# Optimization experiments

Hardware: AMD Instinct MI355X
Metric: run time of the kernel (lower is better)

Reference implementation:

```python
import jax, jax.numpy as jnp
import numpy as np

N = 8192
D = 768
TEMPERATURE = 0.1
EPS_NORM = 1e-8   # torch CosineSimilarity eps
EPS_LOG = 1e-6


def setup_inputs() -> dict:
    key = jax.random.key(0)
    k1, k2, k3 = jax.random.split(key, 3)
    features = jax.random.normal(k1, (N, D), dtype=jnp.float32)
    positive_mask = jax.random.randint(k2, (N, N), 0, 2).astype(jnp.float32)
    negative_mask = jax.random.randint(k3, (N, N), 0, 2).astype(jnp.float32)
    return {"features": features, "positive_mask": positive_mask, "negative_mask": negative_mask}


def reference(features, positive_mask, negative_mask):
    n = features.shape[0]
    # cosine similarity: normalize then GEMM (same math as broadcasted CosineSimilarity)
    norms = jnp.linalg.norm(features, axis=1, keepdims=True)
    fn = features / jnp.maximum(norms, EPS_NORM)
    sim = jnp.exp(jnp.matmul(fn, fn.T) / TEMPERATURE)  # [N, N]
    # zero out self-contrast on the diagonal of both masks
    not_eye = 1.0 - jnp.eye(n, dtype=features.dtype)
    pm = positive_mask * not_eye
    nm = negative_mask * not_eye
    pos_sums = pm.sum(axis=1)
    pos_sums = jnp.where(pos_sums == 0, 1.0, pos_sums)
    neg = jnp.sum(sim * nm, axis=1, keepdims=True)  # [N, 1]
    log_prob = -jnp.log(sim / neg + EPS_LOG)        # [N, N]
    per_row = jnp.sum(log_prob * pm, axis=1) / pos_sums
    return jnp.mean(per_row)
```

## Files before the change

### kernel.cpp

```cpp
#include <hip/hip_runtime.h>
#include <hip/hip_bf16.h>

#define NROWS 8192
#define DDIM 768

typedef short short8 __attribute__((ext_vector_type(8)));
typedef float floatx4 __attribute__((ext_vector_type(4)));
typedef float f4 __attribute__((ext_vector_type(4)));
#define TSTRIDE 132

__global__ __launch_bounds__(256) void normalize_k(const float* __restrict__ f,
                                                   __hip_bfloat16* __restrict__ fn) {
    const int row = blockIdx.x;
    const int t = threadIdx.x;
    const float* fr = f + (size_t)row * DDIM;
    float v0 = fr[t];
    float v1 = fr[t + 256];
    float v2 = fr[t + 512];
    float ss = v0 * v0 + v1 * v1 + v2 * v2;
#pragma unroll
    for (int m = 32; m; m >>= 1) ss += __shfl_xor(ss, m, 64);
    __shared__ float wsum[4];
    if ((t & 63) == 0) wsum[t >> 6] = ss;
    __syncthreads();
    float tot = wsum[0] + wsum[1] + wsum[2] + wsum[3];
    float inv = 1.0f / fmaxf(sqrtf(tot), 1e-8f);
    __hip_bfloat16* o = fn + (size_t)row * DDIM;
    o[t]       = __float2bfloat16(v0 * inv);
    o[t + 256] = __float2bfloat16(v1 * inv);
    o[t + 512] = __float2bfloat16(v2 * inv);
}

__global__ __launch_bounds__(256, 3) void ntxent_main(
        const __hip_bfloat16* __restrict__ fn,
        const float* __restrict__ pmask, const float* __restrict__ nmask,
        float* __restrict__ negG, float* __restrict__ sG,
        float* __restrict__ pG) {
    __shared__ __align__(16) char smem[53248];
    __hip_bfloat16* Is = (__hip_bfloat16*)smem;
    __hip_bfloat16* Js = Is + 128 * 32;
    char* maskLds = smem + 16384;
    float* T = (float*)smem;

    const int t = threadIdx.x;
    const int lane = t & 63;
    const int wv = t >> 6;
    const int wm = wv & 1;
    const int wn = wv >> 1;
    const int q  = lane >> 4;
    const int cl = lane & 15;

    const int bt0 = blockIdx.x;
    const int bt = (bt0 & 7) * 260 + (bt0 >> 3);

    int r = (int)((sqrtf(8.0f * (float)bt + 1.0f) - 1.0f) * 0.5f);
    while ((r + 1) * (r + 2) / 2 <= bt) ++r;
    while (r * (r + 1) / 2 > bt) --r;
    const int c = bt - r * (r + 1) / 2;
    const int rowBase = c * 128;
    const int colBase = r * 128;
    const bool offDiag = (c != r);

    const int rdSw = ((q ^ ((cl >> 1) & 3)) << 4);

    const int sRow = t >> 5;
    const int sChunk = (t & 31) ^ (sRow & 7);

    floatx4 acc[4][4];
#pragma unroll
    for (int mf = 0; mf < 4; ++mf)
#pragma unroll
        for (int nf = 0; nf < 4; ++nf)
            acc[mf][nf] = (floatx4){0.f, 0.f, 0.f, 0.f};

    unsigned int dw[4] = {0u, 0u, 0u, 0u};
    unsigned int mw[4] = {0u, 0u, 0u, 0u};

    auto issue_slab = [&](int s) {
        const int slot = s % 9;
        const int side = s >> 5;
        const int rg   = (s & 31) >> 1;
        const float* mp = (s & 1) ? nmask : pmask;
        const int rowG = (side ? colBase : rowBase) + rg * 8 + sRow;
        const int colG = (side ? rowBase : colBase) + sChunk * 4;
        const float* src = mp + (size_t)rowG * NROWS + colG;
        __builtin_amdgcn_global_load_lds(
            (const __attribute__((address_space(1))) void*)src,
            (__attribute__((address_space(3))) void*)(maskLds + slot * 4096 + t * 16),
            16, 0, 0);
    };

    auto pack_slab = [&](int s) {
        const int slot = s % 9;
        const int side = s >> 5;
        const int rg   = (s & 31) >> 1;
        const int sh   = (s & 1) ? 16 : 0;
        if (side == 0) {
            if (wn == (rg >> 3) && (cl >> 3) == (rg & 1)) {
                const int nf = (rg >> 1) & 3;
                const int rl = cl & 7;
                const char* base = maskLds + slot * 4096 + rl * 512;
                float word = 0.f;
#pragma unroll
                for (int mf = 3; mf >= 0; --mf) {
                    const int pos = (wm * 16 + mf * 4 + q) ^ rl;
                    const f4 m = *(const f4*)(base + pos * 16);
                    float nib = fmaf(2.f, m[1], m[0]) + fmaf(8.f, m[3], 4.f * m[2]);
                    word = fmaf(word, 16.f, nib);
                }
                dw[nf] |= ((unsigned int)word) << sh;
            }
        } else if (offDiag) {
            if (wv == (rg & 3)) {
                const int st = rg >> 2;
                const int rl = (t >> 3) & 7;
                const int h  = t & 7;
                const char* base = maskLds + slot * 4096 + rl * 512;
                float word = 0.f;
#pragma unroll
                for (int u = 3; u >= 0; --u) {
                    const int pos = (h * 4 + u) ^ rl;
                    const f4 m = *(const f4*)(base + pos * 16);
                    float nib = fmaf(2.f, m[1], m[0]) + fmaf(8.f, m[3], 4.f * m[2]);
                    word = fmaf(word, 16.f, nib);
                }
                mw[st] |= ((unsigned int)word) << sh;
            }
        }
    };

    issue_slab(0); issue_slab(1); issue_slab(2);
    issue_slab(3); issue_slab(4); issue_slab(5);
    asm volatile("s_waitcnt vmcnt(3)" ::: "memory");

#pragma unroll
    for (int kt = 0; kt < 24; ++kt) {
        const int k0 = kt * 32;
        asm volatile("s_waitcnt lgkmcnt(0)\n\ts_barrier" ::: "memory");

#pragma unroll
        for (int it = 0; it < 2; ++it) {
            const int s = it * 256 + t;
            const int rr = s >> 2;
            const int cg = (s & 3) ^ ((rr >> 1) & 3);
            const __hip_bfloat16* ga = fn + (size_t)(rowBase + rr) * DDIM + k0 + cg * 8;
            const __hip_bfloat16* gb = fn + (size_t)(colBase + rr) * DDIM + k0 + cg * 8;
            __builtin_amdgcn_global_load_lds(
                (const __attribute__((address_space(1))) void*)ga,
                (__attribute__((address_space(3))) void*)((char*)Is + s * 16), 16, 0, 0);
            __builtin_amdgcn_global_load_lds(
                (const __attribute__((address_space(1))) void*)gb,
                (__attribute__((address_space(3))) void*)((char*)Js + s * 16), 16, 0, 0);
        }

#pragma unroll
        for (int gl = 0; gl < 3; ++gl) {
            const int s = 3 * (kt + 2) + gl;
            if (s <= 63) issue_slab(s);
        }

#pragma unroll
        for (int gl = 0; gl < 3; ++gl) {
            const int s = 3 * kt + gl;
            if (s <= 63) pack_slab(s);
        }

        if (kt <= 18)      asm volatile("s_waitcnt vmcnt(3)\n\ts_barrier" ::: "memory");
        else if (kt == 19) asm volatile("s_waitcnt vmcnt(1)\n\ts_barrier" ::: "memory");
        else               asm volatile("s_waitcnt vmcnt(0)\n\ts_barrier" ::: "memory");

        short8 if_[4];
#pragma unroll
        for (int nf = 0; nf < 4; ++nf) {
            const int rr = wn * 64 + nf * 16 + cl;
            if_[nf] = *(const short8*)((const char*)Is + rr * 64 + rdSw);
        }
#pragma unroll
        for (int mf = 0; mf < 4; ++mf) {
            const int rr = wm * 64 + mf * 16 + cl;
            const short8 jf = *(const short8*)((const char*)Js + rr * 64 + rdSw);
#pragma unroll
            for (int nf = 0; nf < 4; ++nf)
                acc[mf][nf] = __builtin_amdgcn_mfma_f32_16x16x32_bf16(
                    jf, if_[nf], acc[mf][nf], 0, 0, 0);
        }
    }

    const int col64 = colBase + wm * 64;
    const int jb0 = col64 + q * 4;
#pragma unroll
    for (int nf = 0; nf < 4; ++nf) {
        const int grow = rowBase + wn * 64 + nf * 16 + cl;
        const unsigned int w = dw[nf];
        float aN = 0.f, aS = 0.f, aP = 0.f;
#pragma unroll
        for (int mf = 0; mf < 4; ++mf) {
            const int jbase = jb0 + mf * 16;
#pragma unroll
            for (int reg = 0; reg < 4; ++reg) {
                const int b = mf * 4 + reg;
                float pmv = ((w >> b) & 1u) ? 1.0f : 0.0f;
                float nmv = ((w >> (16 + b)) & 1u) ? 1.0f : 0.0f;
                if (grow == jbase + reg) { pmv = 0.f; nmv = 0.f; }
                float v = acc[mf][nf][reg];
                float e = __builtin_amdgcn_exp2f(v * 14.4269504089f);
                aN = fmaf(nmv, e, aN);
                aS = fmaf(pmv, v, aS);
                aP += pmv;
            }
        }
        aN += __shfl_xor(aN, 16, 64);  aN += __shfl_xor(aN, 32, 64);
        aS += __shfl_xor(aS, 16, 64);  aS += __shfl_xor(aS, 32, 64);
        aP += __shfl_xor(aP, 16, 64);  aP += __shfl_xor(aP, 32, 64);
        if (q == 0) {
            atomicAdd(&negG[grow], aN);
            atomicAdd(&sG[grow],   aS);
            atomicAdd(&pG[grow],   aP);
        }
    }

    if (offDiag) {
        const int jl2 = t >> 3;
        const int iseg = (t & 7) * 16;
#pragma unroll
        for (int st = 0; st < 4; ++st) {
            __syncthreads();
            if (wm == (st >> 1)) {
#pragma unroll
                for (int m2 = 0; m2 < 2; ++m2) {
                    const int mf = (st & 1) * 2 + m2;
#pragma unroll
                    for (int nf = 0; nf < 4; ++nf) {
                        const int i = wn * 64 + nf * 16 + cl;
#pragma unroll
                        for (int reg = 0; reg < 4; ++reg) {
                            const int jl = m2 * 16 + q * 4 + reg;
                            T[jl * TSTRIDE + i] = acc[mf][nf][reg];
                        }
                    }
                }
            }
            __syncthreads();
            const int jg = colBase + st * 32 + jl2;
            const unsigned int w = mw[st];
            const f4* tv = (const f4*)(T + jl2 * TSTRIDE + iseg);
            float aN = 0.f, aS = 0.f, aP = 0.f;
#pragma unroll
            for (int u = 0; u < 4; ++u) {
                f4 v4 = tv[u];
#pragma unroll
                for (int e = 0; e < 4; ++e) {
                    const int b = u * 4 + e;
                    float v = v4[e];
                    float pmv = ((w >> b) & 1u) ? 1.0f : 0.0f;
                    float nmv = ((w >> (16 + b)) & 1u) ? 1.0f : 0.0f;
                    float ex = __builtin_amdgcn_exp2f(v * 14.4269504089f);
                    aN = fmaf(nmv, ex, aN);
                    aS = fmaf(pmv, v, aS);
                    aP += pmv;
                }
            }
            aN += __shfl_xor(aN, 1, 64); aN += __shfl_xor(aN, 2, 64); aN += __shfl_xor(aN, 4, 64);
            aS += __shfl_xor(aS, 1, 64); aS += __shfl_xor(aS, 2, 64); aS += __shfl_xor(aS, 4, 64);
            aP += __shfl_xor(aP, 1, 64); aP += __shfl_xor(aP, 2, 64); aP += __shfl_xor(aP, 4, 64);
            if ((t & 7) == 0) {
                atomicAdd(&negG[jg], aN);
                atomicAdd(&sG[jg],   aS);
                atomicAdd(&pG[jg],   aP);
            }
        }
    }
}

__global__ __launch_bounds__(1024) void final_k(const float* __restrict__ negG,
        const float* __restrict__ sG, const float* __restrict__ pG,
        float* __restrict__ out) {
    const int t = threadIdx.x;
    float sum = 0.f;
    for (int i = t; i < NROWS; i += 1024) {
        float P = pG[i];
        if (P > 0.f) {
            sum += (P * logf(negG[i]) - 10.0f * sG[i]) / P;
        }
    }
#pragma unroll
    for (int m = 32; m; m >>= 1) sum += __shfl_xor(sum, m, 64);
    __shared__ float wsum[16];
    if ((t & 63) == 0) wsum[t >> 6] = sum;
    __syncthreads();
    if (t < 16) {
        float v = wsum[t];
#pragma unroll
        for (int m = 8; m; m >>= 1) v += __shfl_xor(v, m, 16);
        if (t == 0) out[0] = v / (float)NROWS;
    }
}

extern "C" void kernel_launch(void* const* d_in, const int* in_sizes, int n_in,
                              void* d_out, int out_size, void* d_ws, size_t ws_size,
                              hipStream_t stream) {
    const float* feat  = (const float*)d_in[0];
    const float* pmask = (const float*)d_in[1];
    const float* nmask = (const float*)d_in[2];
    float* out = (float*)d_out;

    char* ws = (char*)d_ws;
    __hip_bfloat16* fn = (__hip_bfloat16*)ws;
    float* negG = (float*)(ws + 12582912);
    float* sG = negG + NROWS;
    float* pG = sG + NROWS;

    hipMemsetAsync(negG, 0, 3 * NROWS * sizeof(float), stream);

    normalize_k<<<NROWS, 256, 0, stream>>>(feat, fn);

    ntxent_main<<<2080, 256, 0, stream>>>(fn, pmask, nmask, negG, sG, pG);

    final_k<<<1, 1024, 0, stream>>>(negG, sG, pG, out);
}
```

Baseline: 573.4 us.

## Enlarge symmetric tiles to 256x256 with 512-thread blocks and rebalanced mask pipeline

Each block now covers a 256x256 tile of the upper-triangular similarity matrix instead of 128x128. It uses 8 waves, larger accumulators (4x8 MFMA fragments per wave) and a 128KB LDS footprint. The mask slab prefetch schedule is reworked to spread 128 slabs evenly over the 24 K-steps through a 12-slot ring, and slab packing now runs after the MFMAs. The aim is to halve per-tile feature reloads and cut the block count and atomic traffic. The cost is fewer blocks (528), only 2 per CU at most, and heavier register and LDS pressure, which may hurt latency hiding and load balance.

```diff
diff --git a/kernel.cpp b/kernel.cpp
--- a/kernel.cpp
+++ b/kernel.cpp
@@ -7,7 +7,9 @@
 typedef short short8 __attribute__((ext_vector_type(8)));
 typedef float floatx4 __attribute__((ext_vector_type(4)));
 typedef float f4 __attribute__((ext_vector_type(4)));
-#define TSTRIDE 132
+#define TSTRIDE2 260
+
+#define SLB(k) (((k) * 128) / 24)
 
 __global__ __launch_bounds__(256) void normalize_k(const float* __restrict__ f,
                                                    __hip_bfloat16* __restrict__ fn) {
@@ -31,75 +33,92 @@
     o[t + 512] = __float2bfloat16(v2 * inv);
 }
 
-__global__ __launch_bounds__(256, 3) void ntxent_main(
+__global__ __launch_bounds__(512, 2) void ntxent_main(
         const __hip_bfloat16* __restrict__ fn,
         const float* __restrict__ pmask, const float* __restrict__ nmask,
         float* __restrict__ negG, float* __restrict__ sG,
         float* __restrict__ pG) {
-    __shared__ __align__(16) char smem[53248];
-    __hip_bfloat16* Is = (__hip_bfloat16*)smem;
-    __hip_bfloat16* Js = Is + 128 * 32;
-    char* maskLds = smem + 16384;
+    __shared__ __align__(16) char smem[131072];
+    char* IsB = smem;
+    char* JsB = smem + 16384;
+    char* maskLds = smem + 32768;
     float* T = (float*)smem;
 
     const int t = threadIdx.x;
     const int lane = t & 63;
     const int wv = t >> 6;
-    const int wm = wv & 1;
-    const int wn = wv >> 1;
+    const int wn = wv & 1;
+    const int wm = wv >> 1;
     const int q  = lane >> 4;
     const int cl = lane & 15;
 
     const int bt0 = blockIdx.x;
-    const int bt = (bt0 & 7) * 260 + (bt0 >> 3);
+    const int bt = (bt0 & 7) * 66 + (bt0 >> 3);
 
     int r = (int)((sqrtf(8.0f * (float)bt + 1.0f) - 1.0f) * 0.5f);
     while ((r + 1) * (r + 2) / 2 <= bt) ++r;
     while (r * (r + 1) / 2 > bt) --r;
     const int c = bt - r * (r + 1) / 2;
-    const int rowBase = c * 128;
-    const int colBase = r * 128;
+    const int rowBase = c * 256;
+    const int colBase = r * 256;
     const bool offDiag = (c != r);
 
     const int rdSw = ((q ^ ((cl >> 1) & 3)) << 4);
 
-    const int sRow = t >> 5;
-    const int sChunk = (t & 31) ^ (sRow & 7);
-
-    floatx4 acc[4][4];
+    const int sRow = t >> 6;
+    const int sChunk = (t & 63) ^ (sRow & 7);
+
+    floatx4 acc[4][8];
 #pragma unroll
     for (int mf = 0; mf < 4; ++mf)
 #pragma unroll
-        for (int nf = 0; nf < 4; ++nf)
+        for (int nf = 0; nf < 8; ++nf)
             acc[mf][nf] = (floatx4){0.f, 0.f, 0.f, 0.f};
 
-    unsigned int dw[4] = {0u, 0u, 0u, 0u};
-    unsigned int mw[4] = {0u, 0u, 0u, 0u};
+    unsigned int dw[8] = {0u,0u,0u,0u,0u,0u,0u,0u};
+    unsigned int mw[8] = {0u,0u,0u,0u,0u,0u,0u,0u};
 
     auto issue_slab = [&](int s) {
-        const int slot = s % 9;
-        const int side = s >> 5;
-        const int rg   = (s & 31) >> 1;
+        const int slot = s % 12;
+        const int side = s >> 6;
+        const int rg   = (s & 63) >> 1;
         const float* mp = (s & 1) ? nmask : pmask;
         const int rowG = (side ? colBase : rowBase) + rg * 8 + sRow;
         const int colG = (side ? rowBase : colBase) + sChunk * 4;
         const float* src = mp + (size_t)rowG * NROWS + colG;
         __builtin_amdgcn_global_load_lds(
             (const __attribute__((address_space(1))) void*)src,
-            (__attribute__((address_space(3))) void*)(maskLds + slot * 4096 + t * 16),
+            (__attribute__((address_space(3))) void*)(maskLds + slot * 8192 + t * 16),
             16, 0, 0);
     };
 
+    auto issue_fn = [&](int k0) {
+#pragma unroll
+        for (int it = 0; it < 2; ++it) {
+            const int s = it * 512 + t;
+            const int rr = s >> 2;
+            const int cg = (s & 3) ^ ((rr >> 1) & 3);
+            const __hip_bfloat16* ga = fn + (size_t)(rowBase + rr) * DDIM + k0 + cg * 8;
+            const __hip_bfloat16* gb = fn + (size_t)(colBase + rr) * DDIM + k0 + cg * 8;
+            __builtin_amdgcn_global_load_lds(
+                (const __attribute__((address_space(1))) void*)ga,
+                (__attribute__((address_space(3))) void*)(IsB + s * 16), 16, 0, 0);
+            __builtin_amdgcn_global_load_lds(
+                (const __attribute__((address_space(1))) void*)gb,
+                (__attribute__((address_space(3))) void*)(JsB + s * 16), 16, 0, 0);
+        }
+    };
+
     auto pack_slab = [&](int s) {
-        const int slot = s % 9;
-        const int side = s >> 5;
-        const int rg   = (s & 31) >> 1;
+        const int slot = s % 12;
+        const int side = s >> 6;
+        const int rg   = (s & 63) >> 1;
         const int sh   = (s & 1) ? 16 : 0;
         if (side == 0) {
-            if (wn == (rg >> 3) && (cl >> 3) == (rg & 1)) {
-                const int nf = (rg >> 1) & 3;
+            if (wn == ((rg >> 4) & 1) && (cl >> 3) == (rg & 1)) {
+                const int nf = (rg >> 1) & 7;
                 const int rl = cl & 7;
-                const char* base = maskLds + slot * 4096 + rl * 512;
+                const char* base = maskLds + slot * 8192 + rl * 1024;
                 float word = 0.f;
 #pragma unroll
                 for (int mf = 3; mf >= 0; --mf) {
@@ -111,15 +130,14 @@
                 dw[nf] |= ((unsigned int)word) << sh;
             }
         } else if (offDiag) {
-            if (wv == (rg & 3)) {
+            if ((t >> 7) == (rg & 3)) {
                 const int st = rg >> 2;
-                const int rl = (t >> 3) & 7;
-                const int h  = t & 7;
-                const char* base = maskLds + slot * 4096 + rl * 512;
+                const int rl = (t >> 4) & 7;
+                const char* base = maskLds + slot * 8192 + rl * 1024;
                 float word = 0.f;
 #pragma unroll
                 for (int u = 3; u >= 0; --u) {
-                    const int pos = (h * 4 + u) ^ rl;
+                    const int pos = ((t & 15) * 4 + u) ^ rl;
                     const f4 m = *(const f4*)(base + pos * 16);
                     float nib = fmaf(2.f, m[1], m[0]) + fmaf(8.f, m[3], 4.f * m[2]);
                     word = fmaf(word, 16.f, nib);
@@ -129,68 +147,52 @@
         }
     };
 
-    issue_slab(0); issue_slab(1); issue_slab(2);
-    issue_slab(3); issue_slab(4); issue_slab(5);
-    asm volatile("s_waitcnt vmcnt(3)" ::: "memory");
+#pragma unroll
+    for (int s = 0; s < SLB(1); ++s) issue_slab(s);
 
 #pragma unroll
     for (int kt = 0; kt < 24; ++kt) {
-        const int k0 = kt * 32;
         asm volatile("s_waitcnt lgkmcnt(0)\n\ts_barrier" ::: "memory");
 
-#pragma unroll
-        for (int it = 0; it < 2; ++it) {
-            const int s = it * 256 + t;
-            const int rr = s >> 2;
-            const int cg = (s & 3) ^ ((rr >> 1) & 3);
-            const __hip_bfloat16* ga = fn + (size_t)(rowBase + rr) * DDIM + k0 + cg * 8;
-            const __hip_bfloat16* gb = fn + (size_t)(colBase + rr) * DDIM + k0 + cg * 8;
-            __builtin_amdgcn_global_load_lds(
-                (const __attribute__((address_space(1))) void*)ga,
-                (__attribute__((address_space(3))) void*)((char*)Is + s * 16), 16, 0, 0);
-            __builtin_amdgcn_global_load_lds(
-                (const __attribute__((address_space(1))) void*)gb,
-                (__attribute__((address_space(3))) void*)((char*)Js + s * 16), 16, 0, 0);
-        }
-
-#pragma unroll
-        for (int gl = 0; gl < 3; ++gl) {
-            const int s = 3 * (kt + 2) + gl;
-            if (s <= 63) issue_slab(s);
-        }
-
-#pragma unroll
-        for (int gl = 0; gl < 3; ++gl) {
-            const int s = 3 * kt + gl;
-            if (s <= 63) pack_slab(s);
-        }
-
-        if (kt <= 18)      asm volatile("s_waitcnt vmcnt(3)\n\ts_barrier" ::: "memory");
-        else if (kt == 19) asm volatile("s_waitcnt vmcnt(1)\n\ts_barrier" ::: "memory");
-        else               asm volatile("s_waitcnt vmcnt(0)\n\ts_barrier" ::: "memory");
-
-        short8 if_[4];
-#pragma unroll
-        for (int nf = 0; nf < 4; ++nf) {
-            const int rr = wn * 64 + nf * 16 + cl;
-            if_[nf] = *(const short8*)((const char*)Is + rr * 64 + rdSw);
+        issue_fn(kt * 32);
+
+#pragma unroll
+        for (int gl = 0; gl < 6; ++gl) {
+            const int s = SLB(kt + 1) + gl;
+            if (s < SLB(kt + 2)) issue_slab(s);
+        }
+
+        if (kt == 23)           asm volatile("s_waitcnt vmcnt(0)\n\ts_barrier" ::: "memory");
+        else if ((kt % 3) == 1) asm volatile("s_waitcnt vmcnt(6)\n\ts_barrier" ::: "memory");
+        else                    asm volatile("s_waitcnt vmcnt(5)\n\ts_barrier" ::: "memory");
+
+        short8 if_[8];
+#pragma unroll
+        for (int nf = 0; nf < 8; ++nf) {
+            const int rr = wn * 128 + nf * 16 + cl;
+            if_[nf] = *(const short8*)(IsB + rr * 64 + rdSw);
         }
 #pragma unroll
         for (int mf = 0; mf < 4; ++mf) {
             const int rr = wm * 64 + mf * 16 + cl;
-            const short8 jf = *(const short8*)((const char*)Js + rr * 64 + rdSw);
-#pragma unroll
-            for (int nf = 0; nf < 4; ++nf)
+            const short8 jf = *(const short8*)(JsB + rr * 64 + rdSw);
+#pragma unroll
+            for (int nf = 0; nf < 8; ++nf)
                 acc[mf][nf] = __builtin_amdgcn_mfma_f32_16x16x32_bf16(
                     jf, if_[nf], acc[mf][nf], 0, 0, 0);
         }
-    }
-
-    const int col64 = colBase + wm * 64;
-    const int jb0 = col64 + q * 4;
-#pragma unroll
-    for (int nf = 0; nf < 4; ++nf) {
-        const int grow = rowBase + wn * 64 + nf * 16 + cl;
+
+#pragma unroll
+        for (int gl = 0; gl < 6; ++gl) {
+            const int s = SLB(kt) + gl;
+            if (s < SLB(kt + 1)) pack_slab(s);
+        }
+    }
+
+    const int jb0 = colBase + wm * 64 + q * 4;
+#pragma unroll
+    for (int nf = 0; nf < 8; ++nf) {
+        const int grow = rowBase + wn * 128 + nf * 16 + cl;
         const unsigned int w = dw[nf];
         float aN = 0.f, aS = 0.f, aP = 0.f;
 #pragma unroll
@@ -220,22 +222,22 @@
     }
 
     if (offDiag) {
-        const int jl2 = t >> 3;
-        const int iseg = (t & 7) * 16;
-#pragma unroll
-        for (int st = 0; st < 4; ++st) {
+        const int jl2 = t >> 4;
+        const int iseg = (t & 15) * 16;
+#pragma unroll
+        for (int st = 0; st < 8; ++st) {
             __syncthreads();
             if (wm == (st >> 1)) {
 #pragma unroll
                 for (int m2 = 0; m2 < 2; ++m2) {
                     const int mf = (st & 1) * 2 + m2;
 #pragma unroll
-                    for (int nf = 0; nf < 4; ++nf) {
-                        const int i = wn * 64 + nf * 16 + cl;
+                    for (int nf = 0; nf < 8; ++nf) {
+                        const int i = wn * 128 + nf * 16 + cl;
 #pragma unroll
                         for (int reg = 0; reg < 4; ++reg) {
                             const int jl = m2 * 16 + q * 4 + reg;
-                            T[jl * TSTRIDE + i] = acc[mf][nf][reg];
+                            T[jl * TSTRIDE2 + i] = acc[mf][nf][reg];
                         }
                     }
                 }
@@ -243,7 +245,7 @@
             __syncthreads();
             const int jg = colBase + st * 32 + jl2;
             const unsigned int w = mw[st];
-            const f4* tv = (const f4*)(T + jl2 * TSTRIDE + iseg);
+            const f4* tv = (const f4*)(T + jl2 * TSTRIDE2 + iseg);
             float aN = 0.f, aS = 0.f, aP = 0.f;
 #pragma unroll
             for (int u = 0; u < 4; ++u) {
@@ -260,10 +262,13 @@
                     aP += pmv;
                 }
             }
-            aN += __shfl_xor(aN, 1, 64); aN += __shfl_xor(aN, 2, 64); aN += __shfl_xor(aN, 4, 64);
-            aS += __shfl_xor(aS, 1, 64); aS += __shfl_xor(aS, 2, 64); aS += __shfl_xor(aS, 4, 64);
-            aP += __shfl_xor(aP, 1, 64); aP += __shfl_xor(aP, 2, 64); aP += __shfl_xor(aP, 4, 64);
-            if ((t & 7) == 0) {
+            aN += __shfl_xor(aN, 1, 64); aN += __shfl_xor(aN, 2, 64);
+            aN += __shfl_xor(aN, 4, 64); aN += __shfl_xor(aN, 8, 64);
+            aS += __shfl_xor(aS, 1, 64); aS += __shfl_xor(aS, 2, 64);
+            aS += __shfl_xor(aS, 4, 64); aS += __shfl_xor(aS, 8, 64);
+            aP += __shfl_xor(aP, 1, 64); aP += __shfl_xor(aP, 2, 64);
+            aP += __shfl_xor(aP, 4, 64); aP += __shfl_xor(aP, 8, 64);
+            if ((t & 15) == 0) {
                 atomicAdd(&negG[jg], aN);
                 atomicAdd(&sG[jg],   aS);
                 atomicAdd(&pG[jg],   aP);
@@ -314,7 +319,7 @@
 
     normalize_k<<<NROWS, 256, 0, stream>>>(feat, fn);
 
-    ntxent_main<<<2080, 256, 0, stream>>>(fn, pmask, nmask, negG, sG, pG);
+    ntxent_main<<<528, 512, 0, stream>>>(fn, pmask, nmask, negG, sG, pG);
 
     final_k<<<1, 1024, 0, stream>>>(negG, sG, pG, out);
 }
```

After: 733.1 us. +27.9%, slower.
